# Performance work log

Hardware: AMD Instinct MI355X
Metric: run time of the kernel (lower is better)

Reference implementation:

```python
import jax, jax.numpy as jnp
import numpy as np

N_NODES = 50000
N_EDGES = 800000
IN_FEAT = 128
HIDDEN = 128
N_CLASSES = 32


def setup_inputs() -> dict:
    key = jax.random.key(0)
    ks = jax.random.split(key, 8)
    x = jax.random.normal(ks[0], (N_NODES, IN_FEAT), dtype=jnp.float32)
    edge_index = jax.random.randint(ks[1], (2, N_EDGES), 0, N_NODES, dtype=jnp.int64)
    def glorot(k, fan_in, fan_out):
        s = jnp.sqrt(2.0 / (fan_in + fan_out)).astype(jnp.float32)
        return jax.random.normal(k, (fan_in, fan_out), dtype=jnp.float32) * s
    W1 = glorot(ks[2], IN_FEAT, 2 * HIDDEN)
    b1 = jnp.zeros((2 * HIDDEN,), dtype=jnp.float32)
    W2 = glorot(ks[3], 2 * HIDDEN, HIDDEN)
    b2 = jnp.zeros((HIDDEN,), dtype=jnp.float32)
    W3 = glorot(ks[4], HIDDEN, N_CLASSES)
    b3 = jnp.zeros((N_CLASSES,), dtype=jnp.float32)
    return {"x": x, "edge_index": edge_index, "W1": W1, "b1": b1,
            "W2": W2, "b2": b2, "W3": W3, "b3": b3}


def _gcn_norm(edge_index, num_nodes):
    # PyG GCNConv default: add self-loops, symmetric normalization D^-1/2 (A+I) D^-1/2
    loops = jnp.arange(num_nodes, dtype=edge_index.dtype)
    src = jnp.concatenate([edge_index[0], loops])
    dst = jnp.concatenate([edge_index[1], loops])
    ones = jnp.ones_like(dst, dtype=jnp.float32)
    deg = jax.ops.segment_sum(ones, dst, num_segments=num_nodes)
    dinv = jnp.where(deg > 0, 1.0 / jnp.sqrt(deg), 0.0)
    norm = dinv[src] * dinv[dst]  # [E + N]
    return src, dst, norm


def _gcn_conv(x, src, dst, norm, W, b, num_nodes):
    h = x @ W                               # [N, out]
    msg = h[src] * norm[:, None]            # gather + per-edge scale, [E+N, out]
    agg = jax.ops.segment_sum(msg, dst, num_segments=num_nodes)  # scatter-add
    return agg + b


def reference(x, edge_index, W1, b1, W2, b2, W3, b3):
    n = x.shape[0]
    src, dst, norm = _gcn_norm(edge_index, n)
    h = jax.nn.relu(_gcn_conv(x, src, dst, norm, W1, b1, n))
    h = jax.nn.relu(_gcn_conv(h, src, dst, norm, W2, b2, n))
    return _gcn_conv(h, src, dst, norm, W3, b3, n)
```

## Files before the change

### kernel.cpp

```cpp
#include <hip/hip_runtime.h>
#include <hip/hip_fp16.h>

#define NN 50000
#define NE 800000
#define NBKT 391
#define P1B 256

typedef __attribute__((ext_vector_type(8))) _Float16 half8v;
typedef __attribute__((ext_vector_type(4))) float f32x4;

static inline size_t align_up(size_t x, size_t a) { return (x + a - 1) & ~(a - 1); }

union U8 {
    ushort4 u;
    __half2 h[2];
};

__device__ __forceinline__ float4 u8_to_f4(ushort4 uu) {
    U8 c;
    c.u = uu;
    float2 f01 = __half22float2(c.h[0]);
    float2 f23 = __half22float2(c.h[1]);
    return make_float4(f01.x, f01.y, f23.x, f23.y);
}

__device__ __forceinline__ ushort4 f4_to_u8(float4 v) {
    U8 c;
    c.h[0] = __floats2half2_rn(v.x, v.y);
    c.h[1] = __floats2half2_rn(v.z, v.w);
    return c.u;
}

__device__ __forceinline__ int detect64(const int* __restrict__ e) {
    int ok = 1;
    for (int k = 1; k < 64; k += 2) ok &= (e[k] == 0);
    return ok;
}

__global__ __launch_bounds__(256) void bucket_hist(const int* __restrict__ e,
                                                   int* __restrict__ gcount,
                                                   int* __restrict__ base, int E) {
    __shared__ int hist[NBKT];
    const int is64 = detect64(e);
    for (int t = threadIdx.x; t < NBKT; t += 256) hist[t] = 0;
    __syncthreads();
    const int chunk = (E + P1B - 1) / P1B;
    const int b0 = blockIdx.x * chunk;
    const int b1 = min(E, b0 + chunk);
    for (int i = b0 + threadIdx.x; i < b1; i += 256) {
        int d = is64 ? e[2 * (E + i)] : e[E + i];
        atomicAdd(&hist[d >> 7], 1);
    }
    __syncthreads();
    for (int t = threadIdx.x; t < NBKT; t += 256)
        base[blockIdx.x * NBKT + t] = atomicAdd(&gcount[t], hist[t]);
}

__global__ __launch_bounds__(512) void bucket_scan(const int* __restrict__ gcount,
                                                   int* __restrict__ bstart, int nb) {
    __shared__ int s[512];
    const int t = threadIdx.x;
    int v = (t < nb) ? gcount[t] : 0;
    s[t] = v;
    __syncthreads();
    for (int off = 1; off < 512; off <<= 1) {
        int tv = (t >= off) ? s[t - off] : 0;
        __syncthreads();
        s[t] += tv;
        __syncthreads();
    }
    if (t < nb) bstart[t] = s[t] - v;
    if (t == 0) bstart[nb] = s[511];
}

__global__ __launch_bounds__(256) void bucket_scatter(const int* __restrict__ e,
                                                      const int* __restrict__ bstart,
                                                      const int* __restrict__ base,
                                                      unsigned* __restrict__ pairs, int E) {
    __shared__ int cur[NBKT];
    const int is64 = detect64(e);
    for (int t = threadIdx.x; t < NBKT; t += 256)
        cur[t] = bstart[t] + base[blockIdx.x * NBKT + t];
    __syncthreads();
    const int chunk = (E + P1B - 1) / P1B;
    const int b0 = blockIdx.x * chunk;
    const int b1 = min(E, b0 + chunk);
    for (int i = b0 + threadIdx.x; i < b1; i += 256) {
        int s = is64 ? e[2 * i] : e[i];
        int d = is64 ? e[2 * (E + i)] : e[E + i];
        int pos = atomicAdd(&cur[d >> 7], 1);
        pairs[pos] = (unsigned)s | ((unsigned)(d & 127) << 16);
    }
}

__global__ __launch_bounds__(256) void bucket_finalize(const unsigned* __restrict__ pairs,
                                                       const int* __restrict__ bstart,
                                                       const float* __restrict__ x,
                                                       int* __restrict__ row_start,
                                                       int* __restrict__ deg_cnt,
                                                       float* __restrict__ dinv,
                                                       unsigned short* __restrict__ csr,
                                                       unsigned short* __restrict__ xh, int n) {
    __shared__ int ldeg[128];
    __shared__ int lscan[128];
    __shared__ int cur[128];
    __shared__ float sdinv[128];
    const int bkt = blockIdx.x;
    const int s0 = bstart[bkt], s1 = bstart[bkt + 1];
    if (threadIdx.x < 128) ldeg[threadIdx.x] = 0;
    __syncthreads();
    for (int i = s0 + threadIdx.x; i < s1; i += 256)
        atomicAdd(&ldeg[pairs[i] >> 16], 1);
    __syncthreads();
    if (threadIdx.x < 128) lscan[threadIdx.x] = ldeg[threadIdx.x];
    __syncthreads();
    for (int off = 1; off < 128; off <<= 1) {
        int v = 0;
        if (threadIdx.x < 128 && threadIdx.x >= off) v = lscan[threadIdx.x - off];
        __syncthreads();
        if (threadIdx.x < 128) lscan[threadIdx.x] += v;
        __syncthreads();
    }
    if (threadIdx.x < 128) {
        int node = (bkt << 7) + threadIdx.x;
        int exc = s0 + lscan[threadIdx.x] - ldeg[threadIdx.x];
        cur[threadIdx.x] = exc;
        float di = rsqrtf((float)(ldeg[threadIdx.x] + 1));
        sdinv[threadIdx.x] = di;
        if (node < n) {
            row_start[node] = exc;
            deg_cnt[node] = ldeg[threadIdx.x];
            dinv[node] = di;
        }
    }
    __syncthreads();
    for (int i = s0 + threadIdx.x; i < s1; i += 256) {
        unsigned pr = pairs[i];
        int pos = atomicAdd(&cur[pr >> 16], 1);
        csr[pos] = (unsigned short)(pr & 0xFFFFu);
    }
    for (int idx = threadIdx.x; idx < 128 * 32; idx += 256) {
        int ln = idx >> 5;
        int c4 = idx & 31;
        int node = (bkt << 7) + ln;
        if (node < n) {
            float4 v = ((const float4*)x)[(size_t)node * 32 + c4];
            float s = sdinv[ln];
            v.x *= s; v.y *= s; v.z *= s; v.w *= s;
            ((ushort4*)xh)[(size_t)node * 32 + c4] = f4_to_u8(v);
        }
    }
}

__global__ void prep_weights_all(const float* __restrict__ W1, const float* __restrict__ W2,
                                 const float* __restrict__ W3,
                                 unsigned short* __restrict__ w1t,
                                 unsigned short* __restrict__ w2t,
                                 unsigned short* __restrict__ w3t,
                                 int* __restrict__ gcount) {
    int i = blockIdx.x * blockDim.x + threadIdx.x;
    if (i < NBKT + 1) gcount[i] = 0;
    const float* W;
    unsigned short* th;
    int K, M, j;
    if (i < 32768)      { W = W1; th = w1t; K = 128; M = 256; j = i; }
    else if (i < 65536) { W = W2; th = w2t; K = 256; M = 128; j = i - 32768; }
    else if (i < 69632) { W = W3; th = w3t; K = 128; M = 32;  j = i - 65536; }
    else return;
    int k = j / M, m = j % M;
    th[(size_t)m * K + k] = __half_as_ushort(__float2half_rn(W[j]));
}

template <int BM, int BN, int WM, int WN, bool BIAS, bool RELU, bool OUTF16, bool SCALE>
__global__ __launch_bounds__(256) void gemm_f16(
    const unsigned short* __restrict__ A,
    const unsigned short* __restrict__ Wt,
    const float* __restrict__ bias, const float* __restrict__ dscale,
    float* __restrict__ Cf, unsigned short* __restrict__ Ch,
    int N, int K, int M) {
    constexpr int KS = 64;
    constexpr int LDA = KS + 8;
    constexpr int WTM = BM / WM;
    constexpr int WTN = BN / WN;
    constexpr int FM = WTM / 16;
    constexpr int FN = WTN / 16;
    __shared__ unsigned short sA[BM][LDA], sW[BN][LDA];

    const int tid = threadIdx.x;
    const int lane = tid & 63;
    const int w = tid >> 6;
    const int wr = w / WN, wc = w % WN;
    const int row0 = blockIdx.y * BM;
    const int col0 = blockIdx.x * BN;

    f32x4 acc[FM][FN];
#pragma unroll
    for (int m = 0; m < FM; ++m)
#pragma unroll
        for (int nn = 0; nn < FN; ++nn) {
            f32x4 z = {0.f, 0.f, 0.f, 0.f};
            acc[m][nn] = z;
        }

    for (int k0 = 0; k0 < K; k0 += KS) {
        for (int idx = tid; idx < BM * KS / 8; idx += 256) {
            int r = idx / (KS / 8);
            int s = idx % (KS / 8);
            int gr = row0 + r;
            int4 va = make_int4(0, 0, 0, 0);
            if (gr < N) va = *(const int4*)&A[(size_t)gr * K + k0 + s * 8];
            *(int4*)&sA[r][s * 8] = va;
        }
        for (int idx = tid; idx < BN * KS / 8; idx += 256) {
            int c = idx / (KS / 8);
            int s = idx % (KS / 8);
            int gc = col0 + c;
            *(int4*)&sW[c][s * 8] = *(const int4*)&Wt[(size_t)gc * K + k0 + s * 8];
        }
        __syncthreads();

        half8v af[FM][2], wf[FN][2];
        const int koff = (lane >> 4) * 8;
        const int rsel = lane & 15;
#pragma unroll
        for (int m = 0; m < FM; ++m) {
            af[m][0] = *(const half8v*)&sA[wr * WTM + m * 16 + rsel][koff];
            af[m][1] = *(const half8v*)&sA[wr * WTM + m * 16 + rsel][32 + koff];
        }
#pragma unroll
        for (int nn = 0; nn < FN; ++nn) {
            wf[nn][0] = *(const half8v*)&sW[wc * WTN + nn * 16 + rsel][koff];
            wf[nn][1] = *(const half8v*)&sW[wc * WTN + nn * 16 + rsel][32 + koff];
        }
#pragma unroll
        for (int m = 0; m < FM; ++m)
#pragma unroll
            for (int nn = 0; nn < FN; ++nn) {
                acc[m][nn] = __builtin_amdgcn_mfma_f32_16x16x32_f16(af[m][0], wf[nn][0], acc[m][nn], 0, 0, 0);
                acc[m][nn] = __builtin_amdgcn_mfma_f32_16x16x32_f16(af[m][1], wf[nn][1], acc[m][nn], 0, 0, 0);
            }
        __syncthreads();
    }

#pragma unroll
    for (int m = 0; m < FM; ++m) {
#pragma unroll
        for (int r = 0; r < 4; ++r) {
            int row = row0 + wr * WTM + m * 16 + (lane >> 4) * 4 + r;
            if (row >= N) continue;
            float rs = SCALE ? dscale[row] : 1.f;
#pragma unroll
            for (int nn = 0; nn < FN; ++nn) {
                int col = col0 + wc * WTN + nn * 16 + (lane & 15);
                float v = acc[m][nn][r];
                if (BIAS) v += bias[col];
                if (RELU) v = fmaxf(v, 0.f);
                if (SCALE) v *= rs;
                if constexpr (OUTF16) {
                    Ch[(size_t)row * M + col] = __half_as_ushort(__float2half_rn(v));
                } else {
                    Cf[(size_t)row * M + col] = v;
                }
            }
        }
    }
}

__device__ __forceinline__ float4 add4(float4 v, float4 a) {
    a.x += v.x; a.y += v.y; a.z += v.z; a.w += v.w;
    return a;
}

template <int F, int NPB, bool BIAS, bool RELU, bool OUTF16>
__global__ __launch_bounds__((F / 4) * NPB) void agg4h(
    const unsigned short* __restrict__ h, const int* __restrict__ row_start,
    const int* __restrict__ deg_cnt, const unsigned short* __restrict__ csr,
    const float* __restrict__ dinv, const float* __restrict__ bias,
    float* __restrict__ outf, unsigned short* __restrict__ outh, int n) {
    constexpr int L = F / 4;
    const int local = threadIdx.x / L;
    const int lane = threadIdx.x % L;
    const int node = blockIdx.x * NPB + local;
    if (node >= n) return;

    const ushort4* __restrict__ h4 = (const ushort4*)h;
    const float di = dinv[node];

    float4 acc = u8_to_f4(h4[(size_t)node * L + lane]);

    const int beg = row_start[node];
    const int num = deg_cnt[node];
    for (int e = 0; e < num; e += 8) {
        int c[8];
        ushort4 raw[8];
#pragma unroll
        for (int u = 0; u < 8; ++u) {
            int idx = min(e + u, num - 1);
            c[u] = csr[beg + idx];
        }
#pragma unroll
        for (int u = 0; u < 8; ++u) raw[u] = h4[(size_t)c[u] * L + lane];
#pragma unroll
        for (int u = 0; u < 8; ++u) {
            float4 v = u8_to_f4(raw[u]);
            if (e + u < num) acc = add4(v, acc);
        }
    }
    acc.x *= di; acc.y *= di; acc.z *= di; acc.w *= di;
    if (BIAS) {
        const float4 b = ((const float4*)bias)[lane];
        acc.x += b.x; acc.y += b.y; acc.z += b.z; acc.w += b.w;
    }
    if (RELU) {
        acc.x = fmaxf(acc.x, 0.f); acc.y = fmaxf(acc.y, 0.f);
        acc.z = fmaxf(acc.z, 0.f); acc.w = fmaxf(acc.w, 0.f);
    }
    if constexpr (OUTF16) {
        ((ushort4*)outh)[(size_t)node * L + lane] = f4_to_u8(acc);
    } else {
        ((float4*)outf)[(size_t)node * L + lane] = acc;
    }
}

extern "C" void kernel_launch(void* const* d_in, const int* in_sizes, int n_in,
                              void* d_out, int out_size, void* d_ws, size_t ws_size,
                              hipStream_t stream) {
    const float* x   = (const float*)d_in[0];
    const int*   eix = (const int*)d_in[1];
    const float* W1  = (const float*)d_in[2];
    const float* b1  = (const float*)d_in[3];
    const float* W2  = (const float*)d_in[4];
    const float* b2  = (const float*)d_in[5];
    const float* W3  = (const float*)d_in[6];
    const float* b3  = (const float*)d_in[7];
    float* out = (float*)d_out;

    const int n = NN, E = NE;

    char* p = (char*)d_ws;
    auto alloc = [&](size_t bytes) { void* r = (void*)p; p += align_up(bytes, 256); return r; };
    int*   deg_cnt   = (int*)alloc((size_t)n * 4);
    float* dinv      = (float*)alloc((size_t)n * 4);
    int*   row_start = (int*)alloc((size_t)n * 4);
    int*   gcount    = (int*)alloc((size_t)(NBKT + 1) * 4);
    int*   bstart    = (int*)alloc((size_t)(NBKT + 1) * 4);
    int*   base      = (int*)alloc((size_t)P1B * NBKT * 4);
    unsigned* pairs  = (unsigned*)alloc((size_t)E * 4);
    unsigned short* csr = (unsigned short*)alloc((size_t)E * 2);
    unsigned short* w1t = (unsigned short*)alloc((size_t)128 * 256 * 2);
    unsigned short* w2t = (unsigned short*)alloc((size_t)256 * 128 * 2);
    unsigned short* w3t = (unsigned short*)alloc((size_t)128 * 32 * 2);
    unsigned short* xh   = (unsigned short*)alloc((size_t)n * 128 * 2);
    unsigned short* agg0 = (unsigned short*)alloc((size_t)n * 128 * 2);
    unsigned short* h1   = (unsigned short*)alloc((size_t)n * 256 * 2);
    unsigned short* h2s  = (unsigned short*)alloc((size_t)n * 128 * 2);
    unsigned short* x3   = (unsigned short*)alloc((size_t)n * 128 * 2);
    unsigned short* h3s  = (unsigned short*)alloc((size_t)n * 32 * 2);
    (void)ws_size; (void)in_sizes; (void)n_in; (void)out_size;

    prep_weights_all<<<(69632 + 255) / 256, 256, 0, stream>>>(
        W1, W2, W3, w1t, w2t, w3t, gcount);

    bucket_hist<<<P1B, 256, 0, stream>>>(eix, gcount, base, E);
    bucket_scan<<<1, 512, 0, stream>>>(gcount, bstart, NBKT);
    bucket_scatter<<<P1B, 256, 0, stream>>>(eix, bstart, base, pairs, E);
    bucket_finalize<<<NBKT, 256, 0, stream>>>(pairs, bstart, x, row_start, deg_cnt,
                                              dinv, csr, xh, n);

    const int RB = (n + 127) / 128;

    agg4h<128, 8, false, false, true><<<(n + 7) / 8, 256, 0, stream>>>(
        xh, row_start, deg_cnt, csr, dinv, nullptr, nullptr, agg0, n);
    gemm_f16<128, 128, 2, 2, true, true, true, false><<<dim3(2, RB), 256, 0, stream>>>(
        agg0, w1t, b1, nullptr, nullptr, h1, n, 128, 256);

    gemm_f16<128, 128, 2, 2, false, false, true, true><<<dim3(1, RB), 256, 0, stream>>>(
        h1, w2t, nullptr, dinv, nullptr, h2s, n, 256, 128);
    agg4h<128, 8, true, true, true><<<(n + 7) / 8, 256, 0, stream>>>(
        h2s, row_start, deg_cnt, csr, dinv, b2, nullptr, x3, n);

    gemm_f16<128, 32, 4, 1, false, false, true, true><<<dim3(1, RB), 256, 0, stream>>>(
        x3, w3t, nullptr, dinv, nullptr, h3s, n, 128, 32);
    agg4h<32, 32, true, false, false><<<(n + 31) / 32, 256, 0, stream>>>(
        h3s, row_start, deg_cnt, csr, dinv, b3, out, nullptr, n);
}
```

Before: 174.6 us.

## Fuse weight prep into histogram, use direct LDS loads with swizzle, unroll aggregation

Folds the weight transpose/convert kernel into the bucket histogram kernel. It also replaces global atomics on bucket counts with a per-column scan in a single-block kernel, removing one launch and the gcount zeroing. The GEMM now loads tiles with global_load_lds into an unpadded, XOR-swizzled shared layout to avoid register staging and bank conflicts. The aggregation loop gathers 16 neighbors per iteration into two accumulators for more memory-level parallelism. Risks: the single-block column scan is serial over 256 rows, direct LDS loads skip zero-fill for out-of-range rows, and the wider unroll raises register pressure.

```diff
diff --git a/kernel.cpp b/kernel.cpp
--- a/kernel.cpp
+++ b/kernel.cpp
@@ -31,6 +31,13 @@
     return c.u;
 }
 
+__device__ __forceinline__ void gload_lds16(const unsigned short* g, unsigned short* l) {
+    __builtin_amdgcn_global_load_lds(
+        (const __attribute__((address_space(1))) unsigned int*)g,
+        (__attribute__((address_space(3))) unsigned int*)l,
+        16, 0, 0);
+}
+
 __device__ __forceinline__ int detect64(const int* __restrict__ e) {
     int ok = 1;
     for (int k = 1; k < 64; k += 2) ok &= (e[k] == 0);
@@ -38,8 +45,14 @@
 }
 
 __global__ __launch_bounds__(256) void bucket_hist(const int* __restrict__ e,
-                                                   int* __restrict__ gcount,
-                                                   int* __restrict__ base, int E) {
+                                                   int* __restrict__ base,
+                                                   const float* __restrict__ W1,
+                                                   const float* __restrict__ W2,
+                                                   const float* __restrict__ W3,
+                                                   unsigned short* __restrict__ w1t,
+                                                   unsigned short* __restrict__ w2t,
+                                                   unsigned short* __restrict__ w3t,
+                                                   int E) {
     __shared__ int hist[NBKT];
     const int is64 = detect64(e);
     for (int t = threadIdx.x; t < NBKT; t += 256) hist[t] = 0;
@@ -51,17 +64,40 @@
         int d = is64 ? e[2 * (E + i)] : e[E + i];
         atomicAdd(&hist[d >> 7], 1);
     }
+    for (int i = blockIdx.x * 256 + threadIdx.x; i < 69632; i += P1B * 256) {
+        const float* W;
+        unsigned short* th;
+        int K, M, j;
+        if (i < 32768)      { W = W1; th = w1t; K = 128; M = 256; j = i; }
+        else if (i < 65536) { W = W2; th = w2t; K = 256; M = 128; j = i - 32768; }
+        else                { W = W3; th = w3t; K = 128; M = 32;  j = i - 65536; }
+        int k = j / M, m = j % M;
+        th[(size_t)m * K + k] = __half_as_ushort(__float2half_rn(W[j]));
+    }
     __syncthreads();
     for (int t = threadIdx.x; t < NBKT; t += 256)
-        base[blockIdx.x * NBKT + t] = atomicAdd(&gcount[t], hist[t]);
-}
-
-__global__ __launch_bounds__(512) void bucket_scan(const int* __restrict__ gcount,
-                                                   int* __restrict__ bstart, int nb) {
+        base[blockIdx.x * NBKT + t] = hist[t];
+}
+
+__global__ __launch_bounds__(512) void colsum_scan(int* __restrict__ base,
+                                                   int* __restrict__ bstart) {
     __shared__ int s[512];
     const int t = threadIdx.x;
-    int v = (t < nb) ? gcount[t] : 0;
-    s[t] = v;
+    int total = 0;
+    if (t < NBKT) {
+        for (int b0 = 0; b0 < P1B; b0 += 8) {
+            int v[8];
+#pragma unroll
+            for (int u = 0; u < 8; ++u) v[u] = base[(size_t)(b0 + u) * NBKT + t];
+#pragma unroll
+            for (int u = 0; u < 8; ++u) {
+                int nv = v[u];
+                base[(size_t)(b0 + u) * NBKT + t] = total;
+                total += nv;
+            }
+        }
+    }
+    s[t] = (t < NBKT) ? total : 0;
     __syncthreads();
     for (int off = 1; off < 512; off <<= 1) {
         int tv = (t >= off) ? s[t - off] : 0;
@@ -69,8 +105,8 @@
         s[t] += tv;
         __syncthreads();
     }
-    if (t < nb) bstart[t] = s[t] - v;
-    if (t == 0) bstart[nb] = s[511];
+    if (t < NBKT) bstart[t] = s[t] - total;
+    if (t == 0) bstart[NBKT] = s[511];
 }
 
 __global__ __launch_bounds__(256) void bucket_scatter(const int* __restrict__ e,
@@ -152,25 +188,6 @@
     }
 }
 
-__global__ void prep_weights_all(const float* __restrict__ W1, const float* __restrict__ W2,
-                                 const float* __restrict__ W3,
-                                 unsigned short* __restrict__ w1t,
-                                 unsigned short* __restrict__ w2t,
-                                 unsigned short* __restrict__ w3t,
-                                 int* __restrict__ gcount) {
-    int i = blockIdx.x * blockDim.x + threadIdx.x;
-    if (i < NBKT + 1) gcount[i] = 0;
-    const float* W;
-    unsigned short* th;
-    int K, M, j;
-    if (i < 32768)      { W = W1; th = w1t; K = 128; M = 256; j = i; }
-    else if (i < 65536) { W = W2; th = w2t; K = 256; M = 128; j = i - 32768; }
-    else if (i < 69632) { W = W3; th = w3t; K = 128; M = 32;  j = i - 65536; }
-    else return;
-    int k = j / M, m = j % M;
-    th[(size_t)m * K + k] = __half_as_ushort(__float2half_rn(W[j]));
-}
-
 template <int BM, int BN, int WM, int WN, bool BIAS, bool RELU, bool OUTF16, bool SCALE>
 __global__ __launch_bounds__(256) void gemm_f16(
     const unsigned short* __restrict__ A,
@@ -179,12 +196,13 @@
     float* __restrict__ Cf, unsigned short* __restrict__ Ch,
     int N, int K, int M) {
     constexpr int KS = 64;
-    constexpr int LDA = KS + 8;
     constexpr int WTM = BM / WM;
     constexpr int WTN = BN / WN;
     constexpr int FM = WTM / 16;
     constexpr int FN = WTN / 16;
-    __shared__ unsigned short sA[BM][LDA], sW[BN][LDA];
+    constexpr int ACH = BM * 8;
+    constexpr int WCH = BN * 8;
+    __shared__ unsigned short sA[BM][KS], sW[BN][KS];
 
     const int tid = threadIdx.x;
     const int lane = tid & 63;
@@ -203,34 +221,39 @@
         }
 
     for (int k0 = 0; k0 < K; k0 += KS) {
-        for (int idx = tid; idx < BM * KS / 8; idx += 256) {
-            int r = idx / (KS / 8);
-            int s = idx % (KS / 8);
+#pragma unroll
+        for (int b = 0; b < ACH; b += 256) {
+            int idx = b + tid;
+            int r = idx >> 3, s = idx & 7;
             int gr = row0 + r;
-            int4 va = make_int4(0, 0, 0, 0);
-            if (gr < N) va = *(const int4*)&A[(size_t)gr * K + k0 + s * 8];
-            *(int4*)&sA[r][s * 8] = va;
-        }
-        for (int idx = tid; idx < BN * KS / 8; idx += 256) {
-            int c = idx / (KS / 8);
-            int s = idx % (KS / 8);
-            int gc = col0 + c;
-            *(int4*)&sW[c][s * 8] = *(const int4*)&Wt[(size_t)gc * K + k0 + s * 8];
+            int sp = s ^ (r & 7);
+            if (gr < N)
+                gload_lds16(&A[(size_t)gr * K + k0 + sp * 8], &sA[0][0] + idx * 8);
+        }
+#pragma unroll
+        for (int b = 0; b < WCH; b += 256) {
+            int idx = b + tid;
+            int r = idx >> 3, s = idx & 7;
+            int gc = col0 + r;
+            int sp = s ^ (r & 7);
+            gload_lds16(&Wt[(size_t)gc * K + k0 + sp * 8], &sW[0][0] + idx * 8);
         }
         __syncthreads();
 
         half8v af[FM][2], wf[FN][2];
-        const int koff = (lane >> 4) * 8;
         const int rsel = lane & 15;
+        const int cb = lane >> 4;
 #pragma unroll
         for (int m = 0; m < FM; ++m) {
-            af[m][0] = *(const half8v*)&sA[wr * WTM + m * 16 + rsel][koff];
-            af[m][1] = *(const half8v*)&sA[wr * WTM + m * 16 + rsel][32 + koff];
+            int rr = wr * WTM + m * 16 + rsel;
+            af[m][0] = *(const half8v*)&sA[rr][((cb) ^ (rr & 7)) * 8];
+            af[m][1] = *(const half8v*)&sA[rr][((cb + 4) ^ (rr & 7)) * 8];
         }
 #pragma unroll
         for (int nn = 0; nn < FN; ++nn) {
-            wf[nn][0] = *(const half8v*)&sW[wc * WTN + nn * 16 + rsel][koff];
-            wf[nn][1] = *(const half8v*)&sW[wc * WTN + nn * 16 + rsel][32 + koff];
+            int rr = wc * WTN + nn * 16 + rsel;
+            wf[nn][0] = *(const half8v*)&sW[rr][((cb) ^ (rr & 7)) * 8];
+            wf[nn][1] = *(const half8v*)&sW[rr][((cb + 4) ^ (rr & 7)) * 8];
         }
 #pragma unroll
         for (int m = 0; m < FM; ++m)
@@ -286,26 +309,33 @@
     const ushort4* __restrict__ h4 = (const ushort4*)h;
     const float di = dinv[node];
 
-    float4 acc = u8_to_f4(h4[(size_t)node * L + lane]);
+    float4 acc0 = u8_to_f4(h4[(size_t)node * L + lane]);
+    float4 acc1 = make_float4(0.f, 0.f, 0.f, 0.f);
 
     const int beg = row_start[node];
     const int num = deg_cnt[node];
-    for (int e = 0; e < num; e += 8) {
-        int c[8];
-        ushort4 raw[8];
-#pragma unroll
-        for (int u = 0; u < 8; ++u) {
+    for (int e = 0; e < num; e += 16) {
+        int c[16];
+        ushort4 raw[16];
+#pragma unroll
+        for (int u = 0; u < 16; ++u) {
             int idx = min(e + u, num - 1);
             c[u] = csr[beg + idx];
         }
 #pragma unroll
-        for (int u = 0; u < 8; ++u) raw[u] = h4[(size_t)c[u] * L + lane];
+        for (int u = 0; u < 16; ++u) raw[u] = h4[(size_t)c[u] * L + lane];
 #pragma unroll
         for (int u = 0; u < 8; ++u) {
             float4 v = u8_to_f4(raw[u]);
-            if (e + u < num) acc = add4(v, acc);
-        }
-    }
+            if (e + u < num) acc0 = add4(v, acc0);
+        }
+#pragma unroll
+        for (int u = 8; u < 16; ++u) {
+            float4 v = u8_to_f4(raw[u]);
+            if (e + u < num) acc1 = add4(v, acc1);
+        }
+    }
+    float4 acc = add4(acc1, acc0);
     acc.x *= di; acc.y *= di; acc.z *= di; acc.w *= di;
     if (BIAS) {
         const float4 b = ((const float4*)bias)[lane];
@@ -342,7 +372,6 @@
     int*   deg_cnt   = (int*)alloc((size_t)n * 4);
     float* dinv      = (float*)alloc((size_t)n * 4);
     int*   row_start = (int*)alloc((size_t)n * 4);
-    int*   gcount    = (int*)alloc((size_t)(NBKT + 1) * 4);
     int*   bstart    = (int*)alloc((size_t)(NBKT + 1) * 4);
     int*   base      = (int*)alloc((size_t)P1B * NBKT * 4);
     unsigned* pairs  = (unsigned*)alloc((size_t)E * 4);
@@ -358,11 +387,8 @@
     unsigned short* h3s  = (unsigned short*)alloc((size_t)n * 32 * 2);
     (void)ws_size; (void)in_sizes; (void)n_in; (void)out_size;
 
-    prep_weights_all<<<(69632 + 255) / 256, 256, 0, stream>>>(
-        W1, W2, W3, w1t, w2t, w3t, gcount);
-
-    bucket_hist<<<P1B, 256, 0, stream>>>(eix, gcount, base, E);
-    bucket_scan<<<1, 512, 0, stream>>>(gcount, bstart, NBKT);
+    bucket_hist<<<P1B, 256, 0, stream>>>(eix, base, W1, W2, W3, w1t, w2t, w3t, E);
+    colsum_scan<<<1, 512, 0, stream>>>(base, bstart);
     bucket_scatter<<<P1B, 256, 0, stream>>>(eix, bstart, base, pairs, E);
     bucket_finalize<<<NBKT, 256, 0, stream>>>(pairs, bstart, x, row_start, deg_cnt,
                                               dinv, csr, xh, n);
```

Measured after the change: 173.3 us. No clear change (-0.7%).
